# Optimization experiments

Hardware: AMD Instinct MI355X
Metric: run time of the kernel (lower is better)

Reference implementation:

```python
import jax, jax.numpy as jnp
import numpy as np

STRIDES = (8, 16, 32)
IMG = 640
REG_MAX = 16
TOPK = 10
ALPHA = 0.5
BETA = 6.0
EPS_IOU = 1e-16


def _make_anchors():
    # anchor centers for all pyramid levels, (N, 2) in pixel coords
    pts = []
    for s in STRIDES:
        h = w = IMG // s
        ys, xs = jnp.meshgrid(jnp.arange(h, dtype=jnp.float32),
                              jnp.arange(w, dtype=jnp.float32), indexing='ij')
        a = (jnp.stack([xs, ys], axis=-1).reshape(-1, 2) + 0.5) * s
        pts.append(a)
    return jnp.concatenate(pts, axis=0)  # (8400, 2)


def _iou_pairwise(pred, gt):
    # pred (B,N,4), gt (B,M,4) -> IoU (B,M,N)
    b1 = pred[:, None, :, :]   # (B,1,N,4)
    b2 = gt[:, :, None, :]     # (B,M,1,4)
    tl = jnp.maximum(b1[..., :2], b2[..., :2])
    br = jnp.minimum(b1[..., 2:], b2[..., 2:])
    wh = jnp.clip(br - tl, 0.0)
    inter = wh[..., 0] * wh[..., 1]
    a1 = (b1[..., 2] - b1[..., 0]) * (b1[..., 3] - b1[..., 1])
    a2 = (b2[..., 2] - b2[..., 0]) * (b2[..., 3] - b2[..., 1])
    return inter / (a1 + a2 - inter + EPS_IOU)


def _iou_1v1(b1, b2):
    # elementwise IoU, both (..., 4)
    tl = jnp.maximum(b1[..., :2], b2[..., :2])
    br = jnp.minimum(b1[..., 2:], b2[..., 2:])
    wh = jnp.clip(br - tl, 0.0)
    inter = wh[..., 0] * wh[..., 1]
    a1 = (b1[..., 2] - b1[..., 0]) * (b1[..., 3] - b1[..., 1])
    a2 = (b2[..., 2] - b2[..., 0]) * (b2[..., 3] - b2[..., 1])
    return inter / (a1 + a2 - inter + EPS_IOU)


def setup_inputs() -> dict:
    key = jax.random.key(0)
    ks = jax.random.split(key, 6)
    B, N, NC, M = 32, 8400, 80, 40
    pred_scores = jax.random.normal(ks[0], (B, N, NC), jnp.float32)
    pred_dist = jax.random.normal(ks[1], (B, N, 4 * REG_MAX), jnp.float32)
    gt_labels = jax.random.randint(ks[2], (B, M, 1), 0, NC, dtype=jnp.int32)
    cxy = jax.random.uniform(ks[3], (B, M, 2), jnp.float32) * 560.0 + 40.0
    wh = jax.random.uniform(ks[4], (B, M, 2), jnp.float32) * 120.0 + 20.0
    gt_bboxes = jnp.concatenate([jnp.clip(cxy - wh / 2, 0.0, float(IMG)),
                                 jnp.clip(cxy + wh / 2, 0.0, float(IMG))], axis=-1)
    dfl_weight = jax.random.normal(ks[5], (REG_MAX,), jnp.float32) * 0.05
    return {"pred_scores": pred_scores, "pred_dist": pred_dist,
            "gt_labels": gt_labels, "gt_bboxes": gt_bboxes,
            "dfl_weight": dfl_weight}


def reference(pred_scores, pred_dist, gt_labels, gt_bboxes, dfl_weight):
    B, N, NC = pred_scores.shape
    M = gt_bboxes.shape[1]
    anchors = _make_anchors()  # (N, 2)

    # DFL: softmax over reg bins, weighted sum with (random-init) conv weight
    prob = jax.nn.softmax(pred_dist.reshape(B, N, 4, REG_MAX), axis=-1)
    ltrb = prob @ dfl_weight                      # (B,N,4)
    pred_bboxes = jnp.concatenate([anchors - ltrb[..., :2],
                                   anchors + ltrb[..., 2:]], axis=-1)  # (B,N,4) xyxy

    # ---- task-aligned assigner (no-grad) ----
    sg = jax.lax.stop_gradient
    sig = jax.nn.sigmoid(sg(pred_scores))         # (B,N,NC)
    labels = gt_labels[..., 0].astype(jnp.int32)  # (B,M)
    sigT = jnp.swapaxes(sig, 1, 2)                # (B,NC,N)
    scores = jnp.take_along_axis(sigT, jnp.broadcast_to(labels[:, :, None], (B, M, N)), axis=1)  # (B,M,N)
    ious = jnp.clip(_iou_pairwise(sg(pred_bboxes), gt_bboxes), 0.0)      # (B,M,N)
    align = scores ** ALPHA * ious ** BETA        # (B,M,N)

    _, topk_idxs = jax.lax.top_k(align, TOPK)     # (B,M,TOPK) over anchors
    mask = jnp.zeros((B * M, N), dtype=align.dtype)
    mask = mask.at[jnp.arange(B * M)[:, None], topk_idxs.reshape(B * M, TOPK)].set(1.0)
    mask = mask.reshape(B, M, N)
    mask = mask * (align > 1e-9).astype(align.dtype)
    max_m = align.max(axis=1)                     # (B,N) best metric per anchor
    mask = mask * (align == max_m[:, None, :]).astype(align.dtype)

    fg_mask = mask.max(axis=1)                    # (B,N) in {0,1}
    tgt_idx = mask.argmax(axis=1)                 # (B,N) assigned gt index
    ts_sum = jnp.maximum(fg_mask.sum(), 1.0)

    # ---- classification targets (vectorized scatter) ----
    asg_labels = jnp.take_along_axis(labels, tgt_idx, axis=1)  # (B,N)
    target_scores = jax.nn.one_hot(asg_labels, NC, dtype=pred_scores.dtype) * (max_m * fg_mask)[..., None]

    x = pred_scores
    bce = jnp.maximum(x, 0.0) - x * target_scores + jnp.log1p(jnp.exp(-jnp.abs(x)))
    loss_cls = bce.sum() / ts_sum

    # ---- box IoU loss on positives (vectorized gather + mask) ----
    gt_asg = jnp.take_along_axis(gt_bboxes, tgt_idx[..., None], axis=1)  # (B,N,4)
    iou1 = _iou_1v1(pred_bboxes, gt_asg)          # (B,N)
    fg = fg_mask.sum()
    loss_box = jnp.where(fg > 0, ((1.0 - iou1) * fg_mask).sum() / fg, 0.0)

    return loss_cls + loss_box * 1.5
```

## Files before the change

kernel.cpp:

```cpp
#include <hip/hip_runtime.h>
#include <cstdint>
#include <cstddef>

#define BB 32
#define NN 8400
#define NCC 80
#define MM 40
#define RM 16
#define TOPKK 10
#define CAP 2048
#define SLOTP 41

__device__ __forceinline__ void anchor_xy(int n, float& ax, float& ay) {
    int s, x, y;
    if (n < 6400)      { s = 8;  y = n / 80;            x = n - y * 80; }
    else if (n < 8000) { int i = n - 6400; s = 16; y = i / 40; x = i - y * 40; }
    else               { int i = n - 8000; s = 32; y = i / 20; x = i - y * 20; }
    ax = ((float)x + 0.5f) * (float)s;
    ay = ((float)y + 0.5f) * (float)s;
}

__global__ __launch_bounds__(256) void k_main(const float* __restrict__ ps,
                                              const float* __restrict__ pd,
                                              const int*   __restrict__ gl,
                                              const float* __restrict__ gb,
                                              const float* __restrict__ w,
                                              float* __restrict__ pbb,
                                              float* __restrict__ maxm,
                                              int*   __restrict__ cnts,
                                              unsigned long long* __restrict__ lists,
                                              float* __restrict__ accum) {
    __shared__ float  sc[128 * SLOTP];
    __shared__ float4 box[128];
    __shared__ float  gtb[MM * 4];
    __shared__ int    glab[MM];
    __shared__ int    slotm[MM];
    __shared__ int    cmap[NCC];
    __shared__ float  cm[256];
    __shared__ float  redf[4];
    const int b  = blockIdx.y;
    const int n0 = blockIdx.x * 128;
    const int t  = threadIdx.x;

    if (t < MM * 4)              gtb[t] = gb[b * MM * 4 + t];
    if (t >= 192 && t < 192+MM)  glab[t - 192] = gl[b * MM + (t - 192)];
    if (t >= 64 && t < 64+NCC)   cmap[t - 64] = 0x7FFFFFFF;
    __syncthreads();
    if (t < MM) atomicMin(&cmap[glab[t]], t);
    __syncthreads();
    if (t < MM) slotm[t] = cmap[glab[t]];

    #pragma unroll
    for (int h = 0; h < 2; h++) {
        int f = t + h * 256;
        int a = f >> 2, side = f & 3;
        int nc = min(n0 + a, NN - 1);
        const float* p = pd + (((size_t)(b * NN + nc)) * 4 + side) * RM;
        float x[RM];
        #pragma unroll
        for (int i = 0; i < 4; i++) {
            float4 v = *(const float4*)(p + i * 4);
            x[i*4+0] = v.x; x[i*4+1] = v.y; x[i*4+2] = v.z; x[i*4+3] = v.w;
        }
        float mx = x[0];
        #pragma unroll
        for (int i = 1; i < RM; i++) mx = fmaxf(mx, x[i]);
        float s = 0.f, d = 0.f;
        #pragma unroll
        for (int i = 0; i < RM; i++) {
            float e = __builtin_amdgcn_exp2f((x[i] - mx) * 1.44269504f);
            s += e; d += e * w[i];
        }
        ((float*)box)[f] = d * __builtin_amdgcn_rcpf(s);
    }
    __syncthreads();
    if (t < 128) {
        int n = n0 + t;
        float ax, ay; anchor_xy(min(n, NN - 1), ax, ay);
        float4 v = box[t];
        float4 pb = make_float4(ax - v.x, ay - v.y, ax + v.z, ay + v.w);
        box[t] = pb;
        if (n < NN) *(float4*)(pbb + (size_t)(b * NN + n) * 4) = pb;
    }

    float4 vv[10];
    #pragma unroll
    for (int k = 0; k < 10; k++) {
        int f = t + k * 256;
        int row = f / 20, c4 = f - row * 20;
        int nc = min(n0 + row, NN - 1);
        vv[k] = *(const float4*)(ps + ((size_t)(b * NN + nc)) * NCC + c4 * 4);
    }
    float sp = 0.f;
    #pragma unroll
    for (int k = 0; k < 10; k++) {
        int f = t + k * 256;
        int row = f / 20, c4 = f - row * 20;
        float vmask = (n0 + row < NN) ? 1.f : 0.f;
        float xs[4] = {vv[k].x, vv[k].y, vv[k].z, vv[k].w};
        #pragma unroll
        for (int j = 0; j < 4; j++) {
            float x = xs[j];
            float e = __builtin_amdgcn_exp2f(-1.44269504f * fabsf(x));
            float r = __builtin_amdgcn_rcpf(1.0f + e);
            sp += vmask * (fmaxf(x, 0.f) + 0.69314718f * __builtin_amdgcn_logf(1.0f + e));
            int sl = cmap[c4 * 4 + j];
            if (sl < MM) sc[row * SLOTP + sl] = (x >= 0.f) ? r : e * r;
        }
    }
    __syncthreads();

    const int nloc = t & 127;
    const int n    = n0 + nloc;
    const int mb   = (t >> 7) * 20;
    const int lane = t & 63;
    const bool valid = (n < NN);
    float cmax = -INFINITY;
    float4 p4 = box[nloc];
    const float px1 = p4.x, py1 = p4.y, px2 = p4.z, py2 = p4.w;
    const float a1 = (px2 - px1) * (py2 - py1);
    #pragma unroll
    for (int j = 0; j < 20; j++) {
        int m = mb + j;
        float gx1 = gtb[m*4+0], gy1 = gtb[m*4+1], gx2 = gtb[m*4+2], gy2 = gtb[m*4+3];
        float a2 = (gx2 - gx1) * (gy2 - gy1);
        float iw = fmaxf(fminf(px2, gx2) - fmaxf(px1, gx1), 0.f);
        float ih = fmaxf(fminf(py2, gy2) - fmaxf(py1, gy1), 0.f);
        float inter = iw * ih;
        float iou = fmaxf(inter * __builtin_amdgcn_rcpf(a1 + a2 - inter + 1e-16f), 0.f);
        float al = 0.f;
        if (valid) {
            float sg = sc[nloc * SLOTP + slotm[m]];
            float i2 = iou * iou;
            al = __builtin_amdgcn_sqrtf(sg) * (i2 * i2 * i2);
        }
        cmax = fmaxf(cmax, al);
        bool pos = valid && (al > 1e-9f);
        unsigned long long msk = __ballot(pos);
        if (msk) {
            int leader = __ffsll((long long)msk) - 1;
            int basev = 0;
            if (lane == leader) basev = atomicAdd(&cnts[b * MM + m], __popcll(msk));
            basev = __shfl(basev, leader);
            if (pos) {
                int ofs = __popcll(msk & ((1ull << lane) - 1ull));
                int idx = basev + ofs;
                if (idx < CAP)
                    lists[((size_t)(b * MM + m)) * CAP + idx] =
                        ((unsigned long long)__float_as_uint(al) << 32) | (unsigned)n;
            }
        }
    }
    cm[t] = cmax;
    __syncthreads();
    if (t < 128 && valid) maxm[(size_t)b * NN + n] = fmaxf(cm[t], cm[t + 128]);

    #pragma unroll
    for (int off = 32; off > 0; off >>= 1) sp += __shfl_down(sp, off);
    if ((t & 63) == 0) redf[t >> 6] = sp;
    __syncthreads();
    if (t == 0) atomicAdd(accum, redf[0] + redf[1] + redf[2] + redf[3]);
}

__global__ __launch_bounds__(64) void k_topk(const unsigned long long* __restrict__ lists,
                                             const int*   __restrict__ cnts,
                                             const float* __restrict__ maxm,
                                             int* __restrict__ tgt) {
    __shared__ unsigned long long keys[CAP];
    __shared__ unsigned long long sel[TOPKK];
    const int bm = blockIdx.x, b = bm / MM, m = bm % MM, t = threadIdx.x;
    int cnt = min(cnts[bm], CAP);
    int kk = min(TOPKK, cnt);
    for (int i = t; i < cnt; i += 64) {
        unsigned long long L = lists[(size_t)bm * CAP + i];
        keys[i] = (L & 0xFFFFFFFF00000000ull) | (0xFFFFFFFFull - (L & 0xFFFFFFFFull));
    }
    __syncthreads();
    for (int p = 0; p < kk; p++) {
        unsigned long long best = 0ull;
        for (int i = t; i < cnt; i += 64) best = keys[i] > best ? keys[i] : best;
        #pragma unroll
        for (int off = 32; off > 0; off >>= 1) {
            unsigned long long o = __shfl_xor(best, off);
            best = o > best ? o : best;
        }
        for (int i = t; i < cnt; i += 64) if (keys[i] == best) keys[i] = 0ull;
        if (t == 0) sel[p] = best;
        __syncthreads();
    }
    if (t < kk) {
        unsigned long long bb = sel[t];
        float v = __uint_as_float((unsigned)(bb >> 32));
        int n = (int)(0xFFFFFFFFull - (bb & 0xFFFFFFFFull));
        if (v == maxm[(size_t)b * NN + n]) atomicMin(&tgt[(size_t)b * NN + n], m);
    }
}

__global__ __launch_bounds__(256) void k_fg(const int*   __restrict__ tgt,
                                            const int*   __restrict__ gl,
                                            const float* __restrict__ gb,
                                            const float* __restrict__ ps,
                                            const float* __restrict__ pbb,
                                            const float* __restrict__ maxm,
                                            float* __restrict__ accum) {
    int i = blockIdx.x * 256 + threadIdx.x;
    int t = threadIdx.x;
    float vdot = 0.f, vbox = 0.f, vfg = 0.f;
    int tg = tgt[i];
    if (tg < MM) {
        int b = i / NN;
        int lab = gl[b * MM + tg];
        float x = ps[(size_t)i * NCC + lab];
        float mm = maxm[i];
        float4 p = *(const float4*)(pbb + (size_t)i * 4);
        const float* g = gb + ((size_t)b * MM + tg) * 4;
        float a1 = (p.z - p.x) * (p.w - p.y);
        float a2 = (g[2] - g[0]) * (g[3] - g[1]);
        float iw = fmaxf(fminf(p.z, g[2]) - fmaxf(p.x, g[0]), 0.f);
        float ih = fmaxf(fminf(p.w, g[3]) - fmaxf(p.y, g[1]), 0.f);
        float inter = iw * ih;
        float iou = inter / (a1 + a2 - inter + 1e-16f);
        vdot = x * mm; vbox = 1.0f - iou; vfg = 1.0f;
    }
    #pragma unroll
    for (int off = 32; off > 0; off >>= 1) {
        vdot += __shfl_down(vdot, off);
        vbox += __shfl_down(vbox, off);
        vfg  += __shfl_down(vfg,  off);
    }
    __shared__ float r[3][4];
    if ((t & 63) == 0) { int wv = t >> 6; r[0][wv] = vdot; r[1][wv] = vbox; r[2][wv] = vfg; }
    __syncthreads();
    if (t < 3) {
        float s = r[t][0] + r[t][1] + r[t][2] + r[t][3];
        if (s != 0.f) atomicAdd(&accum[1 + t], s);
    }
}

__global__ void k_final(const float* __restrict__ accum, float* __restrict__ out) {
    float S0 = accum[0], dot = accum[1], box = accum[2], fg = accum[3];
    float ts = fmaxf(fg, 1.0f);
    float cls = (S0 - dot) / ts;
    float lb = (fg > 0.f) ? box / fg : 0.f;
    out[0] = cls + 1.5f * lb;
}

extern "C" void kernel_launch(void* const* d_in, const int* in_sizes, int n_in,
                              void* d_out, int out_size, void* d_ws, size_t ws_size,
                              hipStream_t stream) {
    const float* ps = (const float*)d_in[0];
    const float* pd = (const float*)d_in[1];
    const int*   gl = (const int*)  d_in[2];
    const float* gb = (const float*)d_in[3];
    const float* w  = (const float*)d_in[4];

    char* ws = (char*)d_ws;
    constexpr size_t PBB_BYTES  = (size_t)BB * NN * 4 * sizeof(float);
    constexpr size_t MAXM_BYTES = (size_t)BB * NN * sizeof(float);
    constexpr size_t TGT_BYTES  = (size_t)BB * NN * sizeof(int);
    constexpr size_t CNT_BYTES  = 8192;

    float* accum = (float*)ws;
    float* pbb   = (float*)(ws + 256);
    float* maxm  = (float*)(ws + 256 + PBB_BYTES);
    int*   tgt   = (int*)  (ws + 256 + PBB_BYTES + MAXM_BYTES);
    int*   cnts  = (int*)  (ws + 256 + PBB_BYTES + MAXM_BYTES + TGT_BYTES);
    unsigned long long* lists =
        (unsigned long long*)(ws + 256 + PBB_BYTES + MAXM_BYTES + TGT_BYTES + CNT_BYTES);

    hipMemsetAsync(accum, 0, 8 * sizeof(float), stream);
    hipMemsetAsync(tgt, 0x7F, TGT_BYTES, stream);
    hipMemsetAsync(cnts, 0, CNT_BYTES, stream);

    dim3 g3((NN + 127) / 128, BB);
    k_main<<<g3, 256, 0, stream>>>(ps, pd, gl, gb, w, pbb, maxm, cnts, lists, accum);
    k_topk<<<BB * MM, 64, 0, stream>>>(lists, cnts, maxm, tgt);
    k_fg<<<BB * NN / 256, 256, 0, stream>>>(tgt, gl, gb, ps, pbb, maxm, accum);
    k_final<<<1, 1, 0, stream>>>(accum, (float*)d_out);
}
```

Before: 198.7 us.

## Store scores as fp16 in LDS, fuse memsets and final kernel, raise occupancy

Stores per-anchor class sigmoid scores in shared memory as half precision and adds an occupancy hint to k_main. The score load is split into two halves to reduce register pressure. The tgt initialisation moves into k_main and the remaining memsets merge into one header clear. k_final is folded into k_fg using a last-block atomic counter. This targets launch overhead and occupancy limits, at the cost of reduced precision in the alignment metric, which may alter top-k assignments.

```diff
diff --git a/kernel.cpp b/kernel.cpp
--- a/kernel.cpp
+++ b/kernel.cpp
@@ -9,7 +9,7 @@
 #define RM 16
 #define TOPKK 10
 #define CAP 2048
-#define SLOTP 41
+#define SLOTP 42
 
 __device__ __forceinline__ void anchor_xy(int n, float& ax, float& ay) {
     int s, x, y;
@@ -20,17 +20,18 @@
     ay = ((float)y + 0.5f) * (float)s;
 }
 
-__global__ __launch_bounds__(256) void k_main(const float* __restrict__ ps,
-                                              const float* __restrict__ pd,
-                                              const int*   __restrict__ gl,
-                                              const float* __restrict__ gb,
-                                              const float* __restrict__ w,
-                                              float* __restrict__ pbb,
-                                              float* __restrict__ maxm,
-                                              int*   __restrict__ cnts,
-                                              unsigned long long* __restrict__ lists,
-                                              float* __restrict__ accum) {
-    __shared__ float  sc[128 * SLOTP];
+__global__ __launch_bounds__(256, 8) void k_main(const float* __restrict__ ps,
+                                                 const float* __restrict__ pd,
+                                                 const int*   __restrict__ gl,
+                                                 const float* __restrict__ gb,
+                                                 const float* __restrict__ w,
+                                                 float* __restrict__ pbb,
+                                                 float* __restrict__ maxm,
+                                                 int*   __restrict__ cnts,
+                                                 unsigned long long* __restrict__ lists,
+                                                 float* __restrict__ accum,
+                                                 int*   __restrict__ tgt) {
+    __shared__ _Float16 sc[128 * SLOTP];
     __shared__ float4 box[128];
     __shared__ float  gtb[MM * 4];
     __shared__ int    glab[MM];
@@ -42,6 +43,8 @@
     const int n0 = blockIdx.x * 128;
     const int t  = threadIdx.x;
 
+    if (t < 128 && n0 + t < NN) tgt[(size_t)b * NN + n0 + t] = 0x7F7F7F7F;
+
     if (t < MM * 4)              gtb[t] = gb[b * MM * 4 + t];
     if (t >= 192 && t < 192+MM)  glab[t - 192] = gl[b * MM + (t - 192)];
     if (t >= 64 && t < 64+NCC)   cmap[t - 64] = 0x7FFFFFFF;
@@ -83,29 +86,32 @@
         if (n < NN) *(float4*)(pbb + (size_t)(b * NN + n) * 4) = pb;
     }
 
-    float4 vv[10];
-    #pragma unroll
-    for (int k = 0; k < 10; k++) {
-        int f = t + k * 256;
-        int row = f / 20, c4 = f - row * 20;
-        int nc = min(n0 + row, NN - 1);
-        vv[k] = *(const float4*)(ps + ((size_t)(b * NN + nc)) * NCC + c4 * 4);
-    }
     float sp = 0.f;
     #pragma unroll
-    for (int k = 0; k < 10; k++) {
-        int f = t + k * 256;
-        int row = f / 20, c4 = f - row * 20;
-        float vmask = (n0 + row < NN) ? 1.f : 0.f;
-        float xs[4] = {vv[k].x, vv[k].y, vv[k].z, vv[k].w};
-        #pragma unroll
-        for (int j = 0; j < 4; j++) {
-            float x = xs[j];
-            float e = __builtin_amdgcn_exp2f(-1.44269504f * fabsf(x));
-            float r = __builtin_amdgcn_rcpf(1.0f + e);
-            sp += vmask * (fmaxf(x, 0.f) + 0.69314718f * __builtin_amdgcn_logf(1.0f + e));
-            int sl = cmap[c4 * 4 + j];
-            if (sl < MM) sc[row * SLOTP + sl] = (x >= 0.f) ? r : e * r;
+    for (int half = 0; half < 2; half++) {
+        float4 vv[5];
+        #pragma unroll
+        for (int k = 0; k < 5; k++) {
+            int f = t + (half * 5 + k) * 256;
+            int row = f / 20, c4 = f - row * 20;
+            int nc = min(n0 + row, NN - 1);
+            vv[k] = *(const float4*)(ps + ((size_t)(b * NN + nc)) * NCC + c4 * 4);
+        }
+        #pragma unroll
+        for (int k = 0; k < 5; k++) {
+            int f = t + (half * 5 + k) * 256;
+            int row = f / 20, c4 = f - row * 20;
+            float vmask = (n0 + row < NN) ? 1.f : 0.f;
+            float xs[4] = {vv[k].x, vv[k].y, vv[k].z, vv[k].w};
+            #pragma unroll
+            for (int j = 0; j < 4; j++) {
+                float x = xs[j];
+                float e = __builtin_amdgcn_exp2f(-1.44269504f * fabsf(x));
+                float r = __builtin_amdgcn_rcpf(1.0f + e);
+                sp += vmask * (fmaxf(x, 0.f) + 0.69314718f * __builtin_amdgcn_logf(1.0f + e));
+                int sl = cmap[c4 * 4 + j];
+                if (sl < MM) sc[row * SLOTP + sl] = (_Float16)((x >= 0.f) ? r : e * r);
+            }
         }
     }
     __syncthreads();
@@ -130,7 +136,7 @@
         float iou = fmaxf(inter * __builtin_amdgcn_rcpf(a1 + a2 - inter + 1e-16f), 0.f);
         float al = 0.f;
         if (valid) {
-            float sg = sc[nloc * SLOTP + slotm[m]];
+            float sg = (float)sc[nloc * SLOTP + slotm[m]];
             float i2 = iou * iou;
             al = __builtin_amdgcn_sqrtf(sg) * (i2 * i2 * i2);
         }
@@ -202,7 +208,8 @@
                                             const float* __restrict__ ps,
                                             const float* __restrict__ pbb,
                                             const float* __restrict__ maxm,
-                                            float* __restrict__ accum) {
+                                            float* __restrict__ accum,
+                                            float* __restrict__ out) {
     int i = blockIdx.x * 256 + threadIdx.x;
     int t = threadIdx.x;
     float vdot = 0.f, vbox = 0.f, vfg = 0.f;
@@ -235,14 +242,21 @@
         float s = r[t][0] + r[t][1] + r[t][2] + r[t][3];
         if (s != 0.f) atomicAdd(&accum[1 + t], s);
     }
-}
-
-__global__ void k_final(const float* __restrict__ accum, float* __restrict__ out) {
-    float S0 = accum[0], dot = accum[1], box = accum[2], fg = accum[3];
-    float ts = fmaxf(fg, 1.0f);
-    float cls = (S0 - dot) / ts;
-    float lb = (fg > 0.f) ? box / fg : 0.f;
-    out[0] = cls + 1.5f * lb;
+    __syncthreads();
+    __threadfence();
+    if (t == 0) {
+        int old = atomicAdd((int*)&accum[7], 1);
+        if (old == (int)gridDim.x - 1) {
+            float S0  = atomicAdd(&accum[0], 0.f);
+            float dot = atomicAdd(&accum[1], 0.f);
+            float box = atomicAdd(&accum[2], 0.f);
+            float fg  = atomicAdd(&accum[3], 0.f);
+            float ts  = fmaxf(fg, 1.0f);
+            float cls = (S0 - dot) / ts;
+            float lb  = (fg > 0.f) ? box / fg : 0.f;
+            out[0] = cls + 1.5f * lb;
+        }
+    }
 }
 
 extern "C" void kernel_launch(void* const* d_in, const int* in_sizes, int n_in,
@@ -255,26 +269,23 @@
     const float* w  = (const float*)d_in[4];
 
     char* ws = (char*)d_ws;
+    constexpr size_t HDR_BYTES  = 8192;
     constexpr size_t PBB_BYTES  = (size_t)BB * NN * 4 * sizeof(float);
     constexpr size_t MAXM_BYTES = (size_t)BB * NN * sizeof(float);
     constexpr size_t TGT_BYTES  = (size_t)BB * NN * sizeof(int);
-    constexpr size_t CNT_BYTES  = 8192;
 
     float* accum = (float*)ws;
-    float* pbb   = (float*)(ws + 256);
-    float* maxm  = (float*)(ws + 256 + PBB_BYTES);
-    int*   tgt   = (int*)  (ws + 256 + PBB_BYTES + MAXM_BYTES);
-    int*   cnts  = (int*)  (ws + 256 + PBB_BYTES + MAXM_BYTES + TGT_BYTES);
+    int*   cnts  = (int*)(ws + 64);
+    float* pbb   = (float*)(ws + HDR_BYTES);
+    float* maxm  = (float*)(ws + HDR_BYTES + PBB_BYTES);
+    int*   tgt   = (int*)  (ws + HDR_BYTES + PBB_BYTES + MAXM_BYTES);
     unsigned long long* lists =
-        (unsigned long long*)(ws + 256 + PBB_BYTES + MAXM_BYTES + TGT_BYTES + CNT_BYTES);
-
-    hipMemsetAsync(accum, 0, 8 * sizeof(float), stream);
-    hipMemsetAsync(tgt, 0x7F, TGT_BYTES, stream);
-    hipMemsetAsync(cnts, 0, CNT_BYTES, stream);
+        (unsigned long long*)(ws + HDR_BYTES + PBB_BYTES + MAXM_BYTES + TGT_BYTES);
+
+    hipMemsetAsync(ws, 0, HDR_BYTES, stream);
 
     dim3 g3((NN + 127) / 128, BB);
-    k_main<<<g3, 256, 0, stream>>>(ps, pd, gl, gb, w, pbb, maxm, cnts, lists, accum);
+    k_main<<<g3, 256, 0, stream>>>(ps, pd, gl, gb, w, pbb, maxm, cnts, lists, accum, tgt);
     k_topk<<<BB * MM, 64, 0, stream>>>(lists, cnts, maxm, tgt);
-    k_fg<<<BB * NN / 256, 256, 0, stream>>>(tgt, gl, gb, ps, pbb, maxm, accum);
-    k_final<<<1, 1, 0, stream>>>(accum, (float*)d_out);
-}
+    k_fg<<<BB * NN / 256, 256, 0, stream>>>(tgt, gl, gb, ps, pbb, maxm, accum, (float*)d_out);
+}
```

Measured after the change: 321.1 us. +61.6%, slower.
